# Optimization experiments

Hardware: AMD Instinct MI355X
Metric: run time of the kernel (lower is better)

The kernel has to match this reference:

```python
import jax, jax.numpy as jnp
import numpy as np

EMBED = 2048
N_EXPERTS = 64
TOP_K = 8


def setup_inputs() -> dict:
    key = jax.random.key(0)
    k_x, k_w, k_b = jax.random.split(key, 3)
    inputs = jax.random.normal(k_x, (8, 4096, EMBED), dtype=jnp.float32)
    # nn.Linear(embed_size, num_experts): weight [E, D], bias [E]
    bound = 1.0 / np.sqrt(EMBED)
    W = jax.random.uniform(k_w, (N_EXPERTS, EMBED), dtype=jnp.float32, minval=-bound, maxval=bound)
    b = jax.random.uniform(k_b, (N_EXPERTS,), dtype=jnp.float32, minval=-bound, maxval=bound)
    return {"inputs": inputs, "W": W, "b": b}


def reference(inputs, W, b):
    # scores: [B, S, E]
    scores = jnp.einsum("bsd,ed->bse", inputs, W) + b
    topk_scores, indices = jax.lax.top_k(scores, TOP_K)  # [B,S,K]
    # scatter topk_scores into a zero mask (non-selected slots stay 0.0)
    onehot = jax.nn.one_hot(indices, N_EXPERTS, dtype=scores.dtype)  # [B,S,K,E]
    mask = jnp.einsum("bske,bsk->bse", onehot, topk_scores)
    router_output = jax.nn.softmax(mask, axis=-1)
    return (router_output, indices)
```

## Files before the change

### kernel.cpp

```cpp
#include <hip/hip_runtime.h>
#include <math.h>

#define N_TOKENS 32768
#define EMBED    2048
#define NEXP     64
#define TOPK     8
#define BM       64
#define BK       64
#define NCH      (EMBED / BK)
#define SCS      65
#define THRESH   1e-4f
#define WELEMS   (NEXP * EMBED)
#define FIXGRID  1024

typedef __attribute__((ext_vector_type(8)))  short short8;
typedef __attribute__((ext_vector_type(4)))  short short4v;
typedef __attribute__((ext_vector_type(16))) float f32x16;

__device__ __forceinline__ unsigned short bf16rne(float f) {
  unsigned int fb = __float_as_uint(f);
  return (unsigned short)((fb + 0x7FFFu + ((fb >> 16) & 1u)) >> 16);
}

__device__ __forceinline__ void cvt4(float4 f, short4v* h, short4v* l) {
  float fs[4] = {f.x, f.y, f.z, f.w};
  short4v hh, ll;
#pragma unroll
  for (int i = 0; i < 4; ++i) {
    unsigned short hr = bf16rne(fs[i]);
    hh[i] = (short)hr;
    float hf = __uint_as_float((unsigned int)hr << 16);
    ll[i] = (short)bf16rne(fs[i] - hf);
  }
  *h = hh; *l = ll;
}

__global__ void split_w(const float* __restrict__ W, short* __restrict__ wh,
                        short* __restrict__ wl) {
  const int T = blockIdx.x * 256 + threadIdx.x;
  const int n = T >> 8, kg8 = T & 255;
  const float4* W4 = (const float4*)W;
  float4 a = W4[n * 512 + kg8 * 2];
  float4 b = W4[n * 512 + kg8 * 2 + 1];
  short4v h0, l0, h1, l1;
  cvt4(a, &h0, &l0); cvt4(b, &h1, &l1);
  short* dh = &wh[(kg8 * 64 + n) * 8];
  short* dl = &wl[(kg8 * 64 + n) * 8];
  *(short4v*)dh = h0; *(short4v*)(dh + 4) = h1;
  *(short4v*)dl = l0; *(short4v*)(dl + 4) = l1;
}

__global__ __launch_bounds__(256, 4)
void router_kernel(const float* __restrict__ x, const short* __restrict__ wh,
                   const short* __restrict__ wl, const float* __restrict__ bias,
                   int* __restrict__ gcnt, int* __restrict__ glist,
                   float* __restrict__ out) {
  __shared__ float4 lx[2][1024];
  float* sc = (float*)&lx[0][0];

  const int tid  = threadIdx.x;
  const int t0   = blockIdx.x * BM;
  const int lane = tid & 63;
  const int w    = tid >> 6;
  const int half = lane >> 5;
  const int r5   = lane & 31;
  const int tw   = (w & 1) * 32;
  const int ew   = (w >> 1) * 32;

  const float4* x4g = (const float4*)x;
  const short8* Bh  = (const short8*)wh;
  const short8* Bl  = (const short8*)wl;
  const int boff = half * 64 + ew + r5;

  const int row16 = tid >> 4;
  const int s4    = tid & 15;
  const int c4sw  = s4 ^ row16;
  const int wbase = (tid & 192);

  f32x16 acc;
#pragma unroll
  for (int i = 0; i < 16; ++i) acc[i] = 0.f;

#pragma unroll
  for (int i = 0; i < 4; ++i) {
    const float4* gp = x4g + (size_t)(t0 + row16 + 16 * i) * (EMBED / 4) + c4sw;
    __builtin_amdgcn_global_load_lds((const void*)gp, (void*)&lx[0][i * 256 + wbase],
                                     16, 0, 0);
  }

  const int arow  = tw + r5;
  const int am    = arow & 15;
  const int abase = (arow >> 4) * 256 + am * 16;

  for (int ch = 0; ch < NCH; ++ch) {
    const int buf = ch & 1;
    __syncthreads();

    if (ch + 1 < NCH) {
#pragma unroll
      for (int i = 0; i < 4; ++i) {
        const float4* gp = x4g + (size_t)(t0 + row16 + 16 * i) * (EMBED / 4)
                               + (ch + 1) * 16 + c4sw;
        __builtin_amdgcn_global_load_lds((const void*)gp,
                                         (void*)&lx[buf ^ 1][i * 256 + wbase], 16, 0, 0);
      }
    }

    short8 bh[4], bl[4];
#pragma unroll
    for (int s = 0; s < 4; ++s) {
      const int bi = (ch * 4 + s) * 128 + boff;
      bh[s] = Bh[bi]; bl[s] = Bl[bi];
    }

#pragma unroll
    for (int s = 0; s < 4; ++s) {
      const int c0 = s * 4 + half * 2;
      float4 fa = lx[buf][abase + (c0 ^ am)];
      float4 fb = lx[buf][abase + ((c0 + 1) ^ am)];
      short4v h0, l0, h1, l1;
      cvt4(fa, &h0, &l0); cvt4(fb, &h1, &l1);
      short8 ah, al;
#pragma unroll
      for (int j = 0; j < 4; ++j) { ah[j] = h0[j]; ah[j + 4] = h1[j];
                                    al[j] = l0[j]; al[j + 4] = l1[j]; }
      acc = __builtin_amdgcn_mfma_f32_32x32x16_bf16(ah, bh[s], acc, 0, 0, 0);
      acc = __builtin_amdgcn_mfma_f32_32x32x16_bf16(ah, bl[s], acc, 0, 0, 0);
      acc = __builtin_amdgcn_mfma_f32_32x32x16_bf16(al, bh[s], acc, 0, 0, 0);
    }
  }

  __syncthreads();

#pragma unroll
  for (int reg = 0; reg < 16; ++reg) {
    const int row = (reg & 3) + 8 * (reg >> 2) + 4 * half;
    sc[(tw + row) * SCS + ew + r5] = acc[reg];
  }
  __syncthreads();

  float* rout = out;
  float* iout = out + (size_t)N_TOKENS * NEXP;
  const float bias_l = bias[lane];

  for (int tb = 0; tb < 4; ++tb) {
    const int tbase = w * 16 + tb * 4;
    float orig[4]; unsigned cur[4];
#pragma unroll
    for (int i = 0; i < 4; ++i) {
      orig[i] = sc[(tbase + i) * SCS + lane] + bias_l;
      unsigned b = __float_as_uint(orig[i]);
      unsigned u = b ^ (((unsigned)((int)b >> 31)) | 0x80000000u);
      cur[i] = (u & 0xFFFFFFC0u) | (63u - (unsigned)lane);
    }
    float m[4], Z[4], ming[4], prev[4], morig[4];
    int myidx[4]; bool sel[4];
#pragma unroll
    for (int i = 0; i < 4; ++i) { sel[i] = false; morig[i] = 0.f; myidx[i] = 0; ming[i] = 1e30f; }

#pragma unroll
    for (int r = 0; r < 9; ++r) {
      unsigned v[4];
#pragma unroll
      for (int i = 0; i < 4; ++i) v[i] = cur[i];
#pragma unroll
      for (int s2 = 1; s2 < 64; s2 <<= 1) {
#pragma unroll
        for (int i = 0; i < 4; ++i) {
          unsigned o = (unsigned)__shfl_xor((int)v[i], s2);
          v[i] = v[i] > o ? v[i] : o;
        }
      }
#pragma unroll
      for (int i = 0; i < 4; ++i) {
        unsigned vb = (v[i] & 0x80000000u) ? (v[i] ^ 0x80000000u) : ~v[i];
        float fv = __uint_as_float(vb);
        if (r == 0) { m[i] = fmaxf(fv, 0.f); Z[i] = 56.f * expf(-m[i]) + expf(fv - m[i]); }
        else {
          ming[i] = fminf(ming[i], prev[i] - fv);
          if (r < 8) Z[i] += expf(fv - m[i]);
        }
        prev[i] = fv;
        if (r < 8) {
          if (lane == r) myidx[i] = 63 - (int)(v[i] & 63u);
          if (cur[i] == v[i]) { sel[i] = true; morig[i] = orig[i]; cur[i] = 0u; }
        }
      }
    }
#pragma unroll
    for (int i = 0; i < 4; ++i) {
      const int t = tbase + i;
      if (ming[i] < THRESH) {
        if (lane == 0) { int p = atomicAdd(gcnt, 1); glist[p] = t0 + t; }
      } else {
        const float p = expf(morig[i] - m[i]) / Z[i];
        rout[(size_t)(t0 + t) * NEXP + lane] = p;
        if (lane < TOPK) iout[(size_t)(t0 + t) * TOPK + lane] = (float)myidx[i];
      }
    }
  }
}

__global__ __launch_bounds__(256, 4)
void fixup_kernel(const float* __restrict__ x, const float* __restrict__ Wf,
                  const float* __restrict__ bias, const int* __restrict__ gcnt,
                  const int* __restrict__ glist, float* __restrict__ out) {
  __shared__ float4 xsh[512];
  __shared__ double sco[NEXP];
  const int tid  = threadIdx.x;
  const int lane = tid & 63;
  const int w    = tid >> 6;
  float* rout = out;
  float* iout = out + (size_t)N_TOKENS * NEXP;
  const int cnt = *gcnt;

  for (int j = blockIdx.x; j < cnt; j += FIXGRID) {
    const int tok = glist[j];
    const float4* xr = (const float4*)x + (size_t)tok * 512;
    xsh[tid] = xr[tid];
    xsh[tid + 256] = xr[tid + 256];
    __syncthreads();

    for (int i = 0; i < 16; ++i) {
      const int e = w * 16 + i;
      const float4* wr = (const float4*)Wf + (size_t)e * 512;
      double a = 0.0;
#pragma unroll
      for (int q = 0; q < 8; ++q) {
        float4 wv = wr[q * 64 + lane];
        float4 xv = xsh[q * 64 + lane];
        a = fma((double)xv.x, (double)wv.x, a);
        a = fma((double)xv.y, (double)wv.y, a);
        a = fma((double)xv.z, (double)wv.z, a);
        a = fma((double)xv.w, (double)wv.w, a);
      }
#pragma unroll
      for (int s2 = 1; s2 < 64; s2 <<= 1) a += __shfl_xor(a, s2);
      if (lane == 0) sco[e] = a + (double)bias[e];
    }
    __syncthreads();

    if (w == 0) {
      const double orig = sco[lane];
      double curd = orig, vals[8];
      int myidx = 0; double mym = 0.0;
#pragma unroll
      for (int r = 0; r < 8; ++r) {
        double v = curd; int id = lane;
#pragma unroll
        for (int s2 = 1; s2 < 64; s2 <<= 1) {
          const double ov = __shfl_xor(v, s2);
          const int    oi = __shfl_xor(id, s2);
          if (ov > v || (ov == v && oi < id)) { v = ov; id = oi; }
        }
        vals[r] = v;
        if (lane == r)  myidx = id;
        if (lane == id) { mym = orig; curd = -1e300; }
      }
      const double md = fmax(vals[0], 0.0);
      double Zd = 56.0 * exp(-md);
#pragma unroll
      for (int r = 0; r < 8; ++r) Zd += exp(vals[r] - md);
      const double p = exp(mym - md) / Zd;
      rout[(size_t)tok * NEXP + lane] = (float)p;
      if (lane < TOPK) iout[(size_t)tok * TOPK + lane] = (float)myidx;
    }
    __syncthreads();
  }
}

extern "C" void kernel_launch(void* const* d_in, const int* in_sizes, int n_in,
                              void* d_out, int out_size, void* d_ws, size_t ws_size,
                              hipStream_t stream) {
  const float* x = (const float*)d_in[0];
  const float* W = (const float*)d_in[1];
  const float* b = (const float*)d_in[2];
  short* wh = (short*)d_ws;
  short* wl = wh + WELEMS;
  int* gcnt  = (int*)(wl + WELEMS);
  int* glist = gcnt + 4;

  hipMemsetAsync(gcnt, 0, 16, stream);
  split_w<<<64, 256, 0, stream>>>(W, wh, wl);
  router_kernel<<<N_TOKENS / BM, 256, 0, stream>>>(x, wh, wl, b, gcnt, glist,
                                                   (float*)d_out);
  fixup_kernel<<<FIXGRID, 256, 0, stream>>>(x, W, b, gcnt, glist, (float*)d_out);
}
```

Before: 469.7 us.

## Load activations directly to registers with split-K across waves, dropping LDS staging

The router GEMM no longer stages x tiles through LDS with double-buffered global_load_lds and barriers per chunk. Each wave now reads its A fragments straight from global memory into registers with one-step prefetch, and covers all 64 experts with two accumulators. The K dimension is split between wave pairs, and the partial sums are reduced through shared memory at the end. This removes per-chunk barriers and LDS traffic, but doubles accumulator registers, lowers launch bounds occupancy to 2, and relies on uncoalesced strided global loads.

```diff
diff --git a/kernel.cpp b/kernel.cpp
--- a/kernel.cpp
+++ b/kernel.cpp
@@ -6,8 +6,6 @@
 #define NEXP     64
 #define TOPK     8
 #define BM       64
-#define BK       64
-#define NCH      (EMBED / BK)
 #define SCS      65
 #define THRESH   1e-4f
 #define WELEMS   (NEXP * EMBED)
@@ -27,6 +25,19 @@
   short4v hh, ll;
 #pragma unroll
   for (int i = 0; i < 4; ++i) {
+    unsigned short hr = bf16rne(fs[i]);
+    hh[i] = (short)hr;
+    float hf = __uint_as_float((unsigned int)hr << 16);
+    ll[i] = (short)bf16rne(fs[i] - hf);
+  }
+  *h = hh; *l = ll;
+}
+
+__device__ __forceinline__ void cvt8(float4 a, float4 b, short8* h, short8* l) {
+  float fs[8] = {a.x, a.y, a.z, a.w, b.x, b.y, b.z, b.w};
+  short8 hh, ll;
+#pragma unroll
+  for (int i = 0; i < 8; ++i) {
     unsigned short hr = bf16rne(fs[i]);
     hh[i] = (short)hr;
     float hf = __uint_as_float((unsigned int)hr << 16);
@@ -50,92 +61,84 @@
   *(short4v*)dl = l0; *(short4v*)(dl + 4) = l1;
 }
 
-__global__ __launch_bounds__(256, 4)
+__global__ __launch_bounds__(256, 2)
 void router_kernel(const float* __restrict__ x, const short* __restrict__ wh,
                    const short* __restrict__ wl, const float* __restrict__ bias,
                    int* __restrict__ gcnt, int* __restrict__ glist,
                    float* __restrict__ out) {
-  __shared__ float4 lx[2][1024];
-  float* sc = (float*)&lx[0][0];
+  __shared__ float part[2][2][64][16];
+  __shared__ float sc[BM * SCS];
 
   const int tid  = threadIdx.x;
   const int t0   = blockIdx.x * BM;
   const int lane = tid & 63;
   const int w    = tid >> 6;
-  const int half = lane >> 5;
-  const int r5   = lane & 31;
-  const int tw   = (w & 1) * 32;
-  const int ew   = (w >> 1) * 32;
-
-  const float4* x4g = (const float4*)x;
-  const short8* Bh  = (const short8*)wh;
-  const short8* Bl  = (const short8*)wl;
-  const int boff = half * 64 + ew + r5;
-
-  const int row16 = tid >> 4;
-  const int s4    = tid & 15;
-  const int c4sw  = s4 ^ row16;
-  const int wbase = (tid & 192);
-
-  f32x16 acc;
-#pragma unroll
-  for (int i = 0; i < 16; ++i) acc[i] = 0.f;
-
-#pragma unroll
-  for (int i = 0; i < 4; ++i) {
-    const float4* gp = x4g + (size_t)(t0 + row16 + 16 * i) * (EMBED / 4) + c4sw;
-    __builtin_amdgcn_global_load_lds((const void*)gp, (void*)&lx[0][i * 256 + wbase],
-                                     16, 0, 0);
-  }
-
-  const int arow  = tw + r5;
-  const int am    = arow & 15;
-  const int abase = (arow >> 4) * 256 + am * 16;
-
-  for (int ch = 0; ch < NCH; ++ch) {
-    const int buf = ch & 1;
-    __syncthreads();
-
-    if (ch + 1 < NCH) {
-#pragma unroll
-      for (int i = 0; i < 4; ++i) {
-        const float4* gp = x4g + (size_t)(t0 + row16 + 16 * i) * (EMBED / 4)
-                               + (ch + 1) * 16 + c4sw;
-        __builtin_amdgcn_global_load_lds((const void*)gp,
-                                         (void*)&lx[buf ^ 1][i * 256 + wbase], 16, 0, 0);
-      }
-    }
-
-    short8 bh[4], bl[4];
-#pragma unroll
-    for (int s = 0; s < 4; ++s) {
-      const int bi = (ch * 4 + s) * 128 + boff;
-      bh[s] = Bh[bi]; bl[s] = Bl[bi];
-    }
-
-#pragma unroll
-    for (int s = 0; s < 4; ++s) {
-      const int c0 = s * 4 + half * 2;
-      float4 fa = lx[buf][abase + (c0 ^ am)];
-      float4 fb = lx[buf][abase + ((c0 + 1) ^ am)];
-      short4v h0, l0, h1, l1;
-      cvt4(fa, &h0, &l0); cvt4(fb, &h1, &l1);
-      short8 ah, al;
-#pragma unroll
-      for (int j = 0; j < 4; ++j) { ah[j] = h0[j]; ah[j + 4] = h1[j];
-                                    al[j] = l0[j]; al[j + 4] = l1[j]; }
-      acc = __builtin_amdgcn_mfma_f32_32x32x16_bf16(ah, bh[s], acc, 0, 0, 0);
-      acc = __builtin_amdgcn_mfma_f32_32x32x16_bf16(ah, bl[s], acc, 0, 0, 0);
-      acc = __builtin_amdgcn_mfma_f32_32x32x16_bf16(al, bh[s], acc, 0, 0, 0);
-    }
-  }
-
+  const int tt   = w & 1;
+  const int kh   = w >> 1;
+  const int m    = lane & 31;
+  const int kq   = lane >> 5;
+
+  const float*  ap = x + (size_t)(t0 + tt * 32 + m) * EMBED + kh * 1024 + kq * 8;
+  const short8* Bh = (const short8*)wh;
+  const short8* Bl = (const short8*)wl;
+  const int     b0 = (kh * 128 + kq) * 64 + m;
+
+  f32x16 acc0, acc1;
+#pragma unroll
+  for (int i = 0; i < 16; ++i) { acc0[i] = 0.f; acc1[i] = 0.f; }
+
+  float4 a0 = *(const float4*)(ap);
+  float4 a1 = *(const float4*)(ap + 4);
+  short8 bh0 = Bh[b0], bl0 = Bl[b0], bh1 = Bh[b0 + 32], bl1 = Bl[b0 + 32];
+
+#pragma unroll 4
+  for (int s = 0; s < 63; ++s) {
+    float4 na0 = *(const float4*)(ap + (s + 1) * 16);
+    float4 na1 = *(const float4*)(ap + (s + 1) * 16 + 4);
+    const int nb = b0 + (s + 1) * 128;
+    short8 nbh0 = Bh[nb], nbl0 = Bl[nb], nbh1 = Bh[nb + 32], nbl1 = Bl[nb + 32];
+
+    short8 ah, al;
+    cvt8(a0, a1, &ah, &al);
+    acc0 = __builtin_amdgcn_mfma_f32_32x32x16_bf16(ah, bh0, acc0, 0, 0, 0);
+    acc0 = __builtin_amdgcn_mfma_f32_32x32x16_bf16(ah, bl0, acc0, 0, 0, 0);
+    acc0 = __builtin_amdgcn_mfma_f32_32x32x16_bf16(al, bh0, acc0, 0, 0, 0);
+    acc1 = __builtin_amdgcn_mfma_f32_32x32x16_bf16(ah, bh1, acc1, 0, 0, 0);
+    acc1 = __builtin_amdgcn_mfma_f32_32x32x16_bf16(ah, bl1, acc1, 0, 0, 0);
+    acc1 = __builtin_amdgcn_mfma_f32_32x32x16_bf16(al, bh1, acc1, 0, 0, 0);
+
+    a0 = na0; a1 = na1; bh0 = nbh0; bl0 = nbl0; bh1 = nbh1; bl1 = nbl1;
+  }
+  {
+    short8 ah, al;
+    cvt8(a0, a1, &ah, &al);
+    acc0 = __builtin_amdgcn_mfma_f32_32x32x16_bf16(ah, bh0, acc0, 0, 0, 0);
+    acc0 = __builtin_amdgcn_mfma_f32_32x32x16_bf16(ah, bl0, acc0, 0, 0, 0);
+    acc0 = __builtin_amdgcn_mfma_f32_32x32x16_bf16(al, bh0, acc0, 0, 0, 0);
+    acc1 = __builtin_amdgcn_mfma_f32_32x32x16_bf16(ah, bh1, acc1, 0, 0, 0);
+    acc1 = __builtin_amdgcn_mfma_f32_32x32x16_bf16(ah, bl1, acc1, 0, 0, 0);
+    acc1 = __builtin_amdgcn_mfma_f32_32x32x16_bf16(al, bh1, acc1, 0, 0, 0);
+  }
+
+  if (kh == 1) {
+#pragma unroll
+    for (int r = 0; r < 4; ++r) {
+      *(float4*)&part[tt][0][lane][r * 4] =
+        make_float4(acc0[r * 4], acc0[r * 4 + 1], acc0[r * 4 + 2], acc0[r * 4 + 3]);
+      *(float4*)&part[tt][1][lane][r * 4] =
+        make_float4(acc1[r * 4], acc1[r * 4 + 1], acc1[r * 4 + 2], acc1[r * 4 + 3]);
+    }
+  }
   __syncthreads();
-
-#pragma unroll
-  for (int reg = 0; reg < 16; ++reg) {
-    const int row = (reg & 3) + 8 * (reg >> 2) + 4 * half;
-    sc[(tw + row) * SCS + ew + r5] = acc[reg];
+  if (kh == 0) {
+#pragma unroll
+    for (int reg = 0; reg < 16; ++reg) {
+      const float s0 = acc0[reg] + part[tt][0][lane][reg];
+      const float s1 = acc1[reg] + part[tt][1][lane][reg];
+      const int row = (reg & 3) + 8 * (reg >> 2) + 4 * kq;
+      sc[(tt * 32 + row) * SCS + m]      = s0;
+      sc[(tt * 32 + row) * SCS + 32 + m] = s1;
+    }
   }
   __syncthreads();
 
@@ -153,7 +156,7 @@
       unsigned u = b ^ (((unsigned)((int)b >> 31)) | 0x80000000u);
       cur[i] = (u & 0xFFFFFFC0u) | (63u - (unsigned)lane);
     }
-    float m[4], Z[4], ming[4], prev[4], morig[4];
+    float mm[4], Z[4], ming[4], prev[4], morig[4];
     int myidx[4]; bool sel[4];
 #pragma unroll
     for (int i = 0; i < 4; ++i) { sel[i] = false; morig[i] = 0.f; myidx[i] = 0; ming[i] = 1e30f; }
@@ -175,10 +178,10 @@
       for (int i = 0; i < 4; ++i) {
         unsigned vb = (v[i] & 0x80000000u) ? (v[i] ^ 0x80000000u) : ~v[i];
         float fv = __uint_as_float(vb);
-        if (r == 0) { m[i] = fmaxf(fv, 0.f); Z[i] = 56.f * expf(-m[i]) + expf(fv - m[i]); }
+        if (r == 0) { mm[i] = fmaxf(fv, 0.f); Z[i] = 56.f * expf(-mm[i]) + expf(fv - mm[i]); }
         else {
           ming[i] = fminf(ming[i], prev[i] - fv);
-          if (r < 8) Z[i] += expf(fv - m[i]);
+          if (r < 8) Z[i] += expf(fv - mm[i]);
         }
         prev[i] = fv;
         if (r < 8) {
@@ -193,7 +196,7 @@
       if (ming[i] < THRESH) {
         if (lane == 0) { int p = atomicAdd(gcnt, 1); glist[p] = t0 + t; }
       } else {
-        const float p = expf(morig[i] - m[i]) / Z[i];
+        const float p = expf(morig[i] - mm[i]) / Z[i];
         rout[(size_t)(t0 + t) * NEXP + lane] = p;
         if (lane < TOPK) iout[(size_t)(t0 + t) * TOPK + lane] = (float)myidx[i];
       }
```

New measurement: 482.1 us. 2.6% more time.
